# Kernel tuning notes

Hardware: AMD Instinct MI355X
Metric: run time of the kernel (lower is better)

Reference implementation:

```python
import jax, jax.numpy as jnp
import numpy as np

EPS = 1e-6
GROUPS = 8


def setup_inputs() -> dict:
    key = jax.random.key(0)
    ks = jax.random.split(key, 8)
    B, C, H, W = 4, 128, 64, 64
    s = 1.0 / np.sqrt(C)
    return {
        "x": jax.random.normal(ks[0], (B, C, H, W), jnp.float32),
        "gn_scale": jnp.ones((C,), jnp.float32),
        "gn_bias": jnp.zeros((C,), jnp.float32),
        "wq": jax.random.normal(ks[1], (C, C), jnp.float32) * s,
        "bq": jnp.zeros((C,), jnp.float32),
        "wk": jax.random.normal(ks[2], (C, C), jnp.float32) * s,
        "bk": jnp.zeros((C,), jnp.float32),
        "wv": jax.random.normal(ks[3], (C, C), jnp.float32) * s,
        "bv": jnp.zeros((C,), jnp.float32),
        "wp": jax.random.normal(ks[4], (C, C), jnp.float32) * s,
        "bp": jnp.zeros((C,), jnp.float32),
    }


def _group_norm(x, scale, bias):
    B, C, H, W = x.shape
    g = x.reshape(B, GROUPS, C // GROUPS, H * W)
    mu = g.mean(axis=(2, 3), keepdims=True)
    var = g.var(axis=(2, 3), keepdims=True)
    g = (g - mu) * jax.lax.rsqrt(var + EPS)
    g = g.reshape(B, C, H, W)
    return g * scale[None, :, None, None] + bias[None, :, None, None]


def reference(x, gn_scale, gn_bias, wq, bq, wk, bk, wv, bv, wp, bp):
    B, C, H, W = x.shape
    N = H * W
    h = _group_norm(x, gn_scale, gn_bias).reshape(B, C, N)
    # 1x1 convs == channel matmuls: (C_out, C_in) x (B, C_in, N)
    q = jnp.einsum('oc,bcn->bon', wq, h) + bq[None, :, None]
    k = jnp.einsum('oc,bcn->bon', wk, h) + bk[None, :, None]
    v = jnp.einsum('oc,bcn->bon', wv, h) + bv[None, :, None]
    # scores: (B, N, N), w[b,n,m] = sum_c q[b,c,n] k[b,c,m]
    w = jnp.einsum('bcn,bcm->bnm', q, k) * (C ** -0.5)
    w = jax.nn.softmax(w, axis=-1)
    # h_[b,c,n] = sum_m w[b,n,m] v[b,c,m]
    h_ = jnp.einsum('bnm,bcm->bcn', w, v)
    out = jnp.einsum('oc,bcn->bon', wp, h_) + bp[None, :, None]
    return x + out.reshape(B, C, H, W)
```

## Files before the change

kernel.cpp:

```cpp
#include <hip/hip_runtime.h>
#include <math.h>

#define B_ 4
#define C_ 128
#define N_ 4096
#define NSPLIT 4
#define MT 32
#define PLD 40
#define HLD 136
#define VTLD 24

typedef float floatx4 __attribute__((ext_vector_type(4)));
typedef short bf16x8 __attribute__((ext_vector_type(8)));

__device__ __forceinline__ ushort f2bf(float f) {
  unsigned u = __float_as_uint(f);
  return (ushort)((u + 0x7FFF + ((u >> 16) & 1)) >> 16);
}
__device__ __forceinline__ float bf2f(ushort u) {
  return __uint_as_float(((unsigned)u) << 16);
}
__device__ __forceinline__ unsigned pkbf(float a, float b) {
  return __builtin_amdgcn_perm(__float_as_uint(a) + 0x8000u,
                               __float_as_uint(b) + 0x8000u, 0x07060302u);
}
__device__ __forceinline__ void gl2lds16(const ushort* g, ushort* l) {
  __builtin_amdgcn_global_load_lds(
      (const __attribute__((address_space(1))) void*)g,
      (__attribute__((address_space(3))) void*)l, 16, 0, 0);
}

__global__ __launch_bounds__(256) void prep_kernel(
    const float* __restrict__ x, float* __restrict__ gstat,
    const float* __restrict__ wq, const float* __restrict__ wk,
    const float* __restrict__ wv, const float* __restrict__ wp,
    ushort* __restrict__ wB) {
  if (blockIdx.x >= 256) {
    int i = (blockIdx.x - 256) * 256 + threadIdx.x;
    int m = i >> 14, j = i & 16383;
    const float* src = (m == 0) ? wq : (m == 1) ? wk : (m == 2) ? wv : wp;
    wB[i] = f2bf(src[j]);
    return;
  }
  int b = blockIdx.x >> 6, g = (blockIdx.x >> 3) & 7, part = blockIdx.x & 7;
  const float4* xp = (const float4*)(x + (size_t)(b * C_ + g * 16) * N_) + part * 2048;
  float s = 0.f, ss = 0.f;
  for (int i = threadIdx.x; i < 2048; i += 256) {
    float4 v = xp[i];
    s += v.x + v.y + v.z + v.w;
    ss += v.x * v.x + v.y * v.y + v.z * v.z + v.w * v.w;
  }
  #pragma unroll
  for (int o = 32; o > 0; o >>= 1) {
    s += __shfl_down(s, o, 64);
    ss += __shfl_down(ss, o, 64);
  }
  __shared__ float rs[4], rss[4];
  int wid = threadIdx.x >> 6, lane = threadIdx.x & 63;
  if (lane == 0) { rs[wid] = s; rss[wid] = ss; }
  __syncthreads();
  if (threadIdx.x == 0) {
    int slot = (b * 8 + g) * 8 + part;
    gstat[slot]       = rs[0] + rs[1] + rs[2] + rs[3];
    gstat[256 + slot] = rss[0] + rss[1] + rss[2] + rss[3];
  }
}

__global__ __launch_bounds__(256) void gnqkv_kernel(
    const float* __restrict__ x, const float* __restrict__ gstat,
    const float* __restrict__ scale, const float* __restrict__ bias,
    const ushort* __restrict__ wB,
    const float* __restrict__ bq, const float* __restrict__ bk,
    const float* __restrict__ bv,
    ushort* __restrict__ qT, ushort* __restrict__ kT, ushort* __restrict__ vB) {
  __shared__ __align__(16) ushort hs[16][HLD];
  __shared__ __align__(16) ushort Qt[16][HLD];
  __shared__ __align__(16) ushort Kt[16][HLD];
  __shared__ __align__(16) ushort Vt[128][VTLD];
  __shared__ float sSc[C_], sBi[C_];
  int tid = threadIdx.x;
  int b = blockIdx.x >> 8;
  int n0 = (blockIdx.x & 255) * 16;
  if (tid < 128) {
    int g = tid >> 4;
    float S = 0.f, SS = 0.f;
    #pragma unroll
    for (int p = 0; p < 8; ++p) {
      S  += gstat[(b * 8 + g) * 8 + p];
      SS += gstat[256 + (b * 8 + g) * 8 + p];
    }
    float mu = S * (1.f / 65536.f);
    float var = SS * (1.f / 65536.f) - mu * mu;
    float rstd = rsqrtf(var + 1e-6f);
    float sc = scale[tid] * rstd;
    sSc[tid] = sc;
    sBi[tid] = bias[tid] - mu * sc;
  }
  __syncthreads();
  #pragma unroll
  for (int k2 = 0; k2 < 2; ++k2) {
    int i = tid + k2 * 256;
    int c = i >> 2, n4 = i & 3;
    float4 v = *(const float4*)(x + (size_t)(b * C_ + c) * N_ + n0 + n4 * 4);
    float sc = sSc[c], bi = sBi[c];
    hs[n4 * 4 + 0][c] = f2bf(v.x * sc + bi);
    hs[n4 * 4 + 1][c] = f2bf(v.y * sc + bi);
    hs[n4 * 4 + 2][c] = f2bf(v.z * sc + bi);
    hs[n4 * 4 + 3][c] = f2bf(v.w * sc + bi);
  }
  __syncthreads();
  int lane = tid & 63, w = tid >> 6;
  int col = lane & 15, quad = lane >> 4;
  int oh = w * 32;
  bf16x8 hf[4];
  #pragma unroll
  for (int kc = 0; kc < 4; ++kc)
    hf[kc] = *(const bf16x8*)&hs[col][kc * 32 + quad * 8];
  const ushort* Wq = wB;
  const ushort* Wk = wB + 16384;
  const ushort* Wv = wB + 32768;
  const float scl = 0.12751879752224991f;
  #pragma unroll
  for (int ot = 0; ot < 2; ++ot) {
    int o0 = oh + ot * 16;
    floatx4 aq = (floatx4)0.f, ak = (floatx4)0.f, av = (floatx4)0.f;
    #pragma unroll
    for (int kc = 0; kc < 4; ++kc) {
      int wo = (o0 + col) * C_ + kc * 32 + quad * 8;
      aq = __builtin_amdgcn_mfma_f32_16x16x32_bf16(*(const bf16x8*)&Wq[wo], hf[kc], aq, 0, 0, 0);
      ak = __builtin_amdgcn_mfma_f32_16x16x32_bf16(*(const bf16x8*)&Wk[wo], hf[kc], ak, 0, 0, 0);
      av = __builtin_amdgcn_mfma_f32_16x16x32_bf16(*(const bf16x8*)&Wv[wo], hf[kc], av, 0, 0, 0);
    }
    float4 bqv = *(const float4*)&bq[o0 + quad * 4];
    float4 bkv = *(const float4*)&bk[o0 + quad * 4];
    float4 bvv = *(const float4*)&bv[o0 + quad * 4];
    uint2 qs = { pkbf((aq[1] + bqv.y) * scl, (aq[0] + bqv.x) * scl),
                 pkbf((aq[3] + bqv.w) * scl, (aq[2] + bqv.z) * scl) };
    uint2 ks = { pkbf(ak[1] + bkv.y, ak[0] + bkv.x),
                 pkbf(ak[3] + bkv.w, ak[2] + bkv.z) };
    *(uint2*)&Qt[col][o0 + quad * 4] = qs;
    *(uint2*)&Kt[col][o0 + quad * 4] = ks;
    float vv[4] = {av[0] + bvv.x, av[1] + bvv.y, av[2] + bvv.z, av[3] + bvv.w};
    #pragma unroll
    for (int r = 0; r < 4; ++r)
      Vt[o0 + quad * 4 + r][col] = f2bf(vv[r]);
  }
  __syncthreads();
  {
    int row = tid >> 4, seg = tid & 15;
    size_t dst = ((size_t)b * N_ + n0 + row) * C_ + seg * 8;
    *(uint4*)(qT + dst) = *(const uint4*)&Qt[row][seg * 8];
    *(uint4*)(kT + dst) = *(const uint4*)&Kt[row][seg * 8];
  }
  {
    int o = tid >> 1, seg = tid & 1;
    *(uint4*)(vB + ((size_t)b * C_ + o) * N_ + n0 + seg * 8) = *(const uint4*)&Vt[o][seg * 8];
  }
}

__global__ __launch_bounds__(256, 3) void attn_kernel(
    const ushort* __restrict__ qT, const ushort* __restrict__ kT,
    const ushort* __restrict__ vB, ushort* __restrict__ Op,
    float* __restrict__ Lv) {
  __shared__ __align__(16) ushort Ks[2][MT * 128];
  __shared__ __align__(16) ushort Vs[2][C_ * MT];
  __shared__ __align__(16) ushort Ps[128 * PLD];
  int qblk = blockIdx.x & 31;
  int sp = (blockIdx.x >> 5) & 3;
  int b = blockIdx.x >> 7;
  int n0 = qblk * 128;
  int tid = threadIdx.x, lane = tid & 63, w = tid >> 6;
  int col = lane & 15, quad = lane >> 4;
  int wu = __builtin_amdgcn_readfirstlane(w);
  const ushort* kTb = kT + (size_t)b * N_ * C_;
  const ushort* vBb = vB + (size_t)b * C_ * N_;

  bf16x8 qf[2][4];
  #pragma unroll
  for (int qt = 0; qt < 2; ++qt)
    #pragma unroll
    for (int kc = 0; kc < 4; ++kc)
      qf[qt][kc] = *(const bf16x8*)(qT + ((size_t)b * N_ + n0 + w * 32 + qt * 16 + col) * C_ + kc * 32 + quad * 8);

  floatx4 Oacc[8][2];
  #pragma unroll
  for (int qt = 0; qt < 8; ++qt)
    #pragma unroll
    for (int ct = 0; ct < 2; ++ct) Oacc[qt][ct] = (floatx4)0.f;
  float lacc[2] = {0.f, 0.f};

  #define STAGE(m0v, buf)                                                              \
    {                                                                                  \
      _Pragma("unroll")                                                                \
      for (int j = 0; j < 2; ++j) {                                                    \
        int inst = wu * 2 + j;                                                         \
        int r = inst * 4 + (lane >> 4);                                                \
        int pos = (lane & 15) ^ (r & 7);                                               \
        gl2lds16(kTb + (size_t)((m0v) + r) * 128 + pos * 8, &Ks[buf][inst * 512]);     \
      }                                                                                \
      _Pragma("unroll")                                                                \
      for (int j = 0; j < 2; ++j) {                                                    \
        int inst = wu * 2 + j;                                                         \
        int c = inst * 16 + (lane >> 2);                                               \
        gl2lds16(vBb + (size_t)c * N_ + (m0v) + (lane & 3) * 8, &Vs[buf][inst * 512]); \
      }                                                                                \
    }

  STAGE(sp * 1024, 0);
  __syncthreads();

  for (int it = 0; it < 1024 / MT; ++it) {
    if (it < 1024 / MT - 1) STAGE(sp * 1024 + (it + 1) * MT, (it + 1) & 1);
    const ushort* KsB = Ks[it & 1];
    const ushort* VsB = Vs[it & 1];

    floatx4 st[2][2];
    #pragma unroll
    for (int mt = 0; mt < 2; ++mt) {
      int row = mt * 16 + col;
      bf16x8 kf[4];
      #pragma unroll
      for (int kc = 0; kc < 4; ++kc)
        kf[kc] = *(const bf16x8*)&KsB[row * 128 + (((4 * kc + quad) ^ (col & 7)) * 8)];
      #pragma unroll
      for (int qt = 0; qt < 2; ++qt) {
        floatx4 acc = (floatx4)0.f;
        #pragma unroll
        for (int kc = 0; kc < 4; ++kc)
          acc = __builtin_amdgcn_mfma_f32_16x16x32_bf16(kf[kc], qf[qt][kc], acc, 0, 0, 0);
        st[qt][mt] = acc;
      }
    }
    #pragma unroll
    for (int qt = 0; qt < 2; ++qt) {
      int prow = (w * 32 + qt * 16 + col) * PLD;
      #pragma unroll
      for (int mt = 0; mt < 2; ++mt) {
        float p0 = exp2f(st[qt][mt][0]);
        float p1 = exp2f(st[qt][mt][1]);
        float p2 = exp2f(st[qt][mt][2]);
        float p3 = exp2f(st[qt][mt][3]);
        uint2 pk = { pkbf(p1, p0), pkbf(p3, p2) };
        *(uint2*)&Ps[prow + mt * 16 + quad * 4] = pk;
        lacc[qt] += (p0 + p1) + (p2 + p3);
      }
    }
    __syncthreads();
    #pragma unroll
    for (int ct = 0; ct < 2; ++ct) {
      bf16x8 vf = *(const bf16x8*)&VsB[(w * 32 + ct * 16 + col) * MT + quad * 8];
      #pragma unroll
      for (int qt = 0; qt < 8; ++qt) {
        bf16x8 pf = *(const bf16x8*)&Ps[(qt * 16 + col) * PLD + quad * 8];
        Oacc[qt][ct] = __builtin_amdgcn_mfma_f32_16x16x32_bf16(pf, vf, Oacc[qt][ct], 0, 0, 0);
      }
    }
    __syncthreads();
  }

  ushort* OpB = Op + (((size_t)sp * B_ + b) * N_ + n0) * C_;
  #pragma unroll
  for (int qt = 0; qt < 8; ++qt)
    #pragma unroll
    for (int ct = 0; ct < 2; ++ct)
      #pragma unroll
      for (int r = 0; r < 4; ++r)
        OpB[(size_t)(qt * 16 + quad * 4 + r) * C_ + w * 32 + ct * 16 + col] = f2bf(Oacc[qt][ct][r]);
  #pragma unroll
  for (int qt = 0; qt < 2; ++qt) {
    float lsum = lacc[qt];
    lsum += __shfl_xor(lsum, 16, 64);
    lsum += __shfl_xor(lsum, 32, 64);
    if (quad == 0) {
      int idx = b * N_ + n0 + w * 32 + qt * 16 + col;
      Lv[(size_t)sp * (B_ * N_) + idx] = lsum;
    }
  }
}

__global__ __launch_bounds__(256) void mergeproj_kernel(
    const ushort* __restrict__ Op, const float* __restrict__ Lv,
    const ushort* __restrict__ wpB, const float* __restrict__ bp,
    const float* __restrict__ x, float* __restrict__ out) {
  __shared__ __align__(16) ushort tile[16 * HLD];
  int tid = threadIdx.x;
  int b = blockIdx.x >> 8;
  int n0 = (blockIdx.x & 255) * 16;
  {
    int n = tid >> 4, cc = tid & 15;
    int nIdx = b * N_ + n0 + n;
    float den = Lv[0 * (B_ * N_) + nIdx] + Lv[1 * (B_ * N_) + nIdx] +
                Lv[2 * (B_ * N_) + nIdx] + Lv[3 * (B_ * N_) + nIdx];
    float inv = 1.f / den;
    float o[8];
    #pragma unroll
    for (int j = 0; j < 8; ++j) o[j] = 0.f;
    #pragma unroll
    for (int sp = 0; sp < NSPLIT; ++sp) {
      uint4 d = *(const uint4*)&Op[((size_t)sp * (B_ * N_) + nIdx) * C_ + cc * 8];
      unsigned dd[4] = {d.x, d.y, d.z, d.w};
      #pragma unroll
      for (int j = 0; j < 4; ++j) {
        o[j * 2]     += bf2f((ushort)(dd[j] & 0xFFFF));
        o[j * 2 + 1] += bf2f((ushort)(dd[j] >> 16));
      }
    }
    uint4 res;
    res.x = pkbf(o[1] * inv, o[0] * inv);
    res.y = pkbf(o[3] * inv, o[2] * inv);
    res.z = pkbf(o[5] * inv, o[4] * inv);
    res.w = pkbf(o[7] * inv, o[6] * inv);
    *(uint4*)&tile[n * HLD + cc * 8] = res;
  }
  __syncthreads();
  int lane = tid & 63, w = tid >> 6;
  int col = lane & 15, quad = lane >> 4;
  int oh = w * 32;
  bf16x8 hf[4];
  #pragma unroll
  for (int kc = 0; kc < 4; ++kc)
    hf[kc] = *(const bf16x8*)&tile[col * HLD + kc * 32 + quad * 8];
  #pragma unroll
  for (int ot = 0; ot < 2; ++ot) {
    int o0 = oh + ot * 16;
    floatx4 acc = (floatx4)0.f;
    #pragma unroll
    for (int kc = 0; kc < 4; ++kc) {
      int wo = (o0 + col) * C_ + kc * 32 + quad * 8;
      acc = __builtin_amdgcn_mfma_f32_16x16x32_bf16(*(const bf16x8*)&wpB[wo], hf[kc], acc, 0, 0, 0);
    }
    float4 bpv = *(const float4*)&bp[o0 + quad * 4];
    float bb[4] = {bpv.x, bpv.y, bpv.z, bpv.w};
    #pragma unroll
    for (int r = 0; r < 4; ++r) {
      size_t idx = ((size_t)b * C_ + o0 + quad * 4 + r) * N_ + n0 + col;
      out[idx] = acc[r] + bb[r] + x[idx];
    }
  }
}

extern "C" void kernel_launch(void* const* d_in, const int* in_sizes, int n_in,
                              void* d_out, int out_size, void* d_ws, size_t ws_size,
                              hipStream_t stream) {
  const float* x        = (const float*)d_in[0];
  const float* gn_scale = (const float*)d_in[1];
  const float* gn_bias  = (const float*)d_in[2];
  const float* wq = (const float*)d_in[3];
  const float* bq = (const float*)d_in[4];
  const float* wk = (const float*)d_in[5];
  const float* bk = (const float*)d_in[6];
  const float* wv = (const float*)d_in[7];
  const float* bv = (const float*)d_in[8];
  const float* wp = (const float*)d_in[9];
  const float* bp = (const float*)d_in[10];
  float* out = (float*)d_out;

  char* ws = (char*)d_ws;
  float*  Lv    = (float*)(ws + 262144);
  ushort* wB    = (ushort*)(ws + 524288);
  float*  gstat = (float*)(ws + 655360);
  ushort* qT    = (ushort*)(ws + (4u << 20));
  ushort* kT    = (ushort*)(ws + (8u << 20));
  ushort* vB    = (ushort*)(ws + (12u << 20));
  ushort* Op    = (ushort*)(ws + (16u << 20));
  ushort* wpB   = wB + 49152;

  prep_kernel<<<512, 256, 0, stream>>>(x, gstat, wq, wk, wv, wp, wB);
  gnqkv_kernel<<<1024, 256, 0, stream>>>(x, gstat, gn_scale, gn_bias, wB, bq, bk, bv, qT, kT, vB);
  attn_kernel<<<512, 256, 0, stream>>>(qT, kT, vB, Op, Lv);
  mergeproj_kernel<<<1024, 256, 0, stream>>>(Op, Lv, wpB, bp, x, out);
}
```

Before: 154.8 us.

## Split attention block work across eight waves and interleave split-K block order

Doubles the attention block to 512 threads (8 waves). Each wave now computes half of the score tile per KV chunk and a 64x32 slice of the output accumulator, instead of a full 32-row slice of both. Row-sum partials from wave pairs are combined through shared memory before being written. The block index mapping also changes so that the four splits of one query block run next to each other. This halves per-wave accumulator registers to raise occupancy and latency hiding, at the cost of redundant Q fragment loads per wave pair and a larger block barrier.

```diff
diff --git a/kernel.cpp b/kernel.cpp
--- a/kernel.cpp
+++ b/kernel.cpp
@@ -158,20 +158,23 @@
   }
 }
 
-__global__ __launch_bounds__(256, 3) void attn_kernel(
+__global__ __launch_bounds__(512, 4) void attn_kernel(
     const ushort* __restrict__ qT, const ushort* __restrict__ kT,
     const ushort* __restrict__ vB, ushort* __restrict__ Op,
     float* __restrict__ Lv) {
   __shared__ __align__(16) ushort Ks[2][MT * 128];
   __shared__ __align__(16) ushort Vs[2][C_ * MT];
   __shared__ __align__(16) ushort Ps[128 * PLD];
-  int qblk = blockIdx.x & 31;
-  int sp = (blockIdx.x >> 5) & 3;
+  __shared__ float lpart[8][2][16];
+  int sp = blockIdx.x & 3;
+  int qblk = (blockIdx.x >> 2) & 31;
   int b = blockIdx.x >> 7;
   int n0 = qblk * 128;
   int tid = threadIdx.x, lane = tid & 63, w = tid >> 6;
   int col = lane & 15, quad = lane >> 4;
   int wu = __builtin_amdgcn_readfirstlane(w);
+  int mtw = w & 1, qg = w >> 1;
+  int qh = w & 1, cq = w >> 1;
   const ushort* kTb = kT + (size_t)b * N_ * C_;
   const ushort* vBb = vB + (size_t)b * C_ * N_;
 
@@ -180,30 +183,22 @@
   for (int qt = 0; qt < 2; ++qt)
     #pragma unroll
     for (int kc = 0; kc < 4; ++kc)
-      qf[qt][kc] = *(const bf16x8*)(qT + ((size_t)b * N_ + n0 + w * 32 + qt * 16 + col) * C_ + kc * 32 + quad * 8);
-
-  floatx4 Oacc[8][2];
-  #pragma unroll
-  for (int qt = 0; qt < 8; ++qt)
+      qf[qt][kc] = *(const bf16x8*)(qT + ((size_t)b * N_ + n0 + qg * 32 + qt * 16 + col) * C_ + kc * 32 + quad * 8);
+
+  floatx4 Oacc[4][2];
+  #pragma unroll
+  for (int qt = 0; qt < 4; ++qt)
     #pragma unroll
     for (int ct = 0; ct < 2; ++ct) Oacc[qt][ct] = (floatx4)0.f;
   float lacc[2] = {0.f, 0.f};
 
-  #define STAGE(m0v, buf)                                                              \
-    {                                                                                  \
-      _Pragma("unroll")                                                                \
-      for (int j = 0; j < 2; ++j) {                                                    \
-        int inst = wu * 2 + j;                                                         \
-        int r = inst * 4 + (lane >> 4);                                                \
-        int pos = (lane & 15) ^ (r & 7);                                               \
-        gl2lds16(kTb + (size_t)((m0v) + r) * 128 + pos * 8, &Ks[buf][inst * 512]);     \
-      }                                                                                \
-      _Pragma("unroll")                                                                \
-      for (int j = 0; j < 2; ++j) {                                                    \
-        int inst = wu * 2 + j;                                                         \
-        int c = inst * 16 + (lane >> 2);                                               \
-        gl2lds16(vBb + (size_t)c * N_ + (m0v) + (lane & 3) * 8, &Vs[buf][inst * 512]); \
-      }                                                                                \
+  #define STAGE(m0v, buf)                                                            \
+    {                                                                                \
+      int r = wu * 4 + (lane >> 4);                                                  \
+      int pos = (lane & 15) ^ (r & 7);                                               \
+      gl2lds16(kTb + (size_t)((m0v) + r) * 128 + pos * 8, &Ks[buf][wu * 512]);       \
+      int c = wu * 16 + (lane >> 2);                                                 \
+      gl2lds16(vBb + (size_t)c * N_ + (m0v) + (lane & 3) * 8, &Vs[buf][wu * 512]);   \
     }
 
   STAGE(sp * 1024, 0);
@@ -214,10 +209,9 @@
     const ushort* KsB = Ks[it & 1];
     const ushort* VsB = Vs[it & 1];
 
-    floatx4 st[2][2];
-    #pragma unroll
-    for (int mt = 0; mt < 2; ++mt) {
-      int row = mt * 16 + col;
+    floatx4 st[2];
+    {
+      int row = mtw * 16 + col;
       bf16x8 kf[4];
       #pragma unroll
       for (int kc = 0; kc < 4; ++kc)
@@ -228,52 +222,57 @@
         #pragma unroll
         for (int kc = 0; kc < 4; ++kc)
           acc = __builtin_amdgcn_mfma_f32_16x16x32_bf16(kf[kc], qf[qt][kc], acc, 0, 0, 0);
-        st[qt][mt] = acc;
+        st[qt] = acc;
       }
     }
     #pragma unroll
     for (int qt = 0; qt < 2; ++qt) {
-      int prow = (w * 32 + qt * 16 + col) * PLD;
-      #pragma unroll
-      for (int mt = 0; mt < 2; ++mt) {
-        float p0 = exp2f(st[qt][mt][0]);
-        float p1 = exp2f(st[qt][mt][1]);
-        float p2 = exp2f(st[qt][mt][2]);
-        float p3 = exp2f(st[qt][mt][3]);
-        uint2 pk = { pkbf(p1, p0), pkbf(p3, p2) };
-        *(uint2*)&Ps[prow + mt * 16 + quad * 4] = pk;
-        lacc[qt] += (p0 + p1) + (p2 + p3);
-      }
+      int prow = (qg * 32 + qt * 16 + col) * PLD + mtw * 16;
+      float p0 = exp2f(st[qt][0]);
+      float p1 = exp2f(st[qt][1]);
+      float p2 = exp2f(st[qt][2]);
+      float p3 = exp2f(st[qt][3]);
+      uint2 pk = { pkbf(p1, p0), pkbf(p3, p2) };
+      *(uint2*)&Ps[prow + quad * 4] = pk;
+      lacc[qt] += (p0 + p1) + (p2 + p3);
     }
     __syncthreads();
-    #pragma unroll
-    for (int ct = 0; ct < 2; ++ct) {
-      bf16x8 vf = *(const bf16x8*)&VsB[(w * 32 + ct * 16 + col) * MT + quad * 8];
-      #pragma unroll
-      for (int qt = 0; qt < 8; ++qt) {
-        bf16x8 pf = *(const bf16x8*)&Ps[(qt * 16 + col) * PLD + quad * 8];
-        Oacc[qt][ct] = __builtin_amdgcn_mfma_f32_16x16x32_bf16(pf, vf, Oacc[qt][ct], 0, 0, 0);
-      }
+    bf16x8 vf[2];
+    #pragma unroll
+    for (int ct = 0; ct < 2; ++ct)
+      vf[ct] = *(const bf16x8*)&VsB[(cq * 32 + ct * 16 + col) * MT + quad * 8];
+    #pragma unroll
+    for (int qt = 0; qt < 4; ++qt) {
+      bf16x8 pf = *(const bf16x8*)&Ps[(qh * 64 + qt * 16 + col) * PLD + quad * 8];
+      #pragma unroll
+      for (int ct = 0; ct < 2; ++ct)
+        Oacc[qt][ct] = __builtin_amdgcn_mfma_f32_16x16x32_bf16(pf, vf[ct], Oacc[qt][ct], 0, 0, 0);
     }
     __syncthreads();
   }
 
   ushort* OpB = Op + (((size_t)sp * B_ + b) * N_ + n0) * C_;
   #pragma unroll
-  for (int qt = 0; qt < 8; ++qt)
+  for (int qt = 0; qt < 4; ++qt)
     #pragma unroll
     for (int ct = 0; ct < 2; ++ct)
       #pragma unroll
       for (int r = 0; r < 4; ++r)
-        OpB[(size_t)(qt * 16 + quad * 4 + r) * C_ + w * 32 + ct * 16 + col] = f2bf(Oacc[qt][ct][r]);
+        OpB[(size_t)(qh * 64 + qt * 16 + quad * 4 + r) * C_ + cq * 32 + ct * 16 + col] =
+            f2bf(Oacc[qt][ct][r]);
   #pragma unroll
   for (int qt = 0; qt < 2; ++qt) {
     float lsum = lacc[qt];
     lsum += __shfl_xor(lsum, 16, 64);
     lsum += __shfl_xor(lsum, 32, 64);
-    if (quad == 0) {
-      int idx = b * N_ + n0 + w * 32 + qt * 16 + col;
-      Lv[(size_t)sp * (B_ * N_) + idx] = lsum;
+    if (quad == 0) lpart[w][qt][col] = lsum;
+  }
+  __syncthreads();
+  if ((w & 1) == 0 && quad == 0) {
+    #pragma unroll
+    for (int qt = 0; qt < 2; ++qt) {
+      int idx = b * N_ + n0 + (w >> 1) * 32 + qt * 16 + col;
+      Lv[(size_t)sp * (B_ * N_) + idx] = lpart[w][qt][col] + lpart[w + 1][qt][col];
     }
   }
 }
@@ -367,6 +366,6 @@
 
   prep_kernel<<<512, 256, 0, stream>>>(x, gstat, wq, wk, wv, wp, wB);
   gnqkv_kernel<<<1024, 256, 0, stream>>>(x, gstat, gn_scale, gn_bias, wB, bq, bk, bv, qT, kT, vB);
-  attn_kernel<<<512, 256, 0, stream>>>(qT, kT, vB, Op, Lv);
+  attn_kernel<<<512, 512, 0, stream>>>(qT, kT, vB, Op, Lv);
   mergeproj_kernel<<<1024, 256, 0, stream>>>(Op, Lv, wpB, bp, x, out);
 }
```

Result: no change. 153.8 us (-0.6%).
